# Performance work log

Measured on AMD Instinct MI355X. Metric: run time of the kernel, lower is better.

Reference implementation:

```python
import jax, jax.numpy as jnp
import numpy as np

B, N, H, OUT, L = 32, 4096, 256, 256, 4
EPS = 1e-5


def _build_edge_index(num_nodes):
    grid = int(np.sqrt(num_nodes)) + 1
    edges = []
    for i in range(num_nodes):
        col = i % grid
        if col < grid - 1 and i + 1 < num_nodes:
            edges.append([i, i + 1]); edges.append([i + 1, i])
        if i + grid < num_nodes:
            edges.append([i, i + grid]); edges.append([i + grid, i])
    return np.asarray(edges, dtype=np.int64).T  # [2, E]


def setup_inputs() -> dict:
    key = jax.random.key(0)
    ks = jax.random.split(key, 12)
    s = 0.02
    x = (jax.random.uniform(ks[0], (B, N)) < 0.1).astype(jnp.float32)  # syndrome bits
    edge_index = jnp.asarray(_build_edge_index(N))
    return {
        "x": x,
        "edge_index": edge_index,
        "proj_w": jax.random.normal(ks[1], (1, H)) * s,
        "proj_b": jnp.zeros((H,)),
        "conv_w": jax.random.normal(ks[2], (L, H, H)) * s,
        "conv_b": jnp.zeros((L, H)),
        "ln_g": jnp.ones((L, H)),
        "ln_b": jnp.zeros((L, H)),
        "h1_w": jax.random.normal(ks[3], (H, H)) * s,
        "h1_b": jnp.zeros((H,)),
        "h2_w": jax.random.normal(ks[4], (H, OUT)) * s,
        "h2_b": jnp.zeros((OUT,)),
    }


def reference(x, edge_index, proj_w, proj_b, conv_w, conv_b, ln_g, ln_b,
              h1_w, h1_b, h2_w, h2_b):
    batch, n = x.shape
    total = batch * n
    # batched edge index: replicate per sample with node offsets
    offsets = (jnp.arange(batch, dtype=edge_index.dtype) * n)
    ei = (edge_index[:, None, :] + offsets[None, :, None]).reshape(2, -1)
    src, dst = ei[0], ei[1]

    h = x.reshape(total, 1) @ proj_w + proj_b  # [total, H]

    # GCN symmetric norm with self-loops (degree = in-degree + 1)
    deg = jnp.zeros((total,), h.dtype).at[dst].add(1.0) + 1.0
    dinv_sqrt = jax.lax.rsqrt(deg)
    enorm = (dinv_sqrt[src] * dinv_sqrt[dst])[:, None]  # [E, 1]
    self_norm = (1.0 / deg)[:, None]                    # [total, 1]

    for l in range(L):
        t = h @ conv_w[l]                                   # transform
        agg = jnp.zeros_like(t).at[dst].add(enorm * t[src])  # scatter-add
        t = agg + self_norm * t + conv_b[l]
        mu = t.mean(-1, keepdims=True)
        var = ((t - mu) ** 2).mean(-1, keepdims=True)
        t = (t - mu) * jax.lax.rsqrt(var + EPS) * ln_g[l] + ln_b[l]
        h = jax.nn.relu(t)

    pooled = h.reshape(batch, n, -1).mean(axis=1)  # global_mean_pool (equal-size graphs)
    return jax.nn.relu(pooled @ h1_w + h1_b) @ h2_w + h2_b
```

## Files before the change

### kernel.cpp

```cpp
#include <hip/hip_runtime.h>
#include <cstdint>
#include <cstddef>

#define TOTAL (32*4096)
#define H 256
#define NLAYER 4

typedef _Float16 f16x8 __attribute__((ext_vector_type(8)));
typedef _Float16 f16x4 __attribute__((ext_vector_type(4)));
typedef float floatx4 __attribute__((ext_vector_type(4)));

__device__ __forceinline__ float dinv_of(int n) {
  int col = n % 65;
  int deg = 1;
  deg += (n >= 1 && col != 0) ? 1 : 0;
  deg += (col != 64 && n <= 4094) ? 1 : 0;
  deg += (n >= 65) ? 1 : 0;
  deg += (n <= 4030) ? 1 : 0;
  return rsqrtf((float)deg);
}

__device__ __forceinline__ void loadf8(const float* p, float* v) {
  float4 a = *reinterpret_cast<const float4*>(p);
  float4 b = *reinterpret_cast<const float4*>(p + 4);
  v[0] = a.x; v[1] = a.y; v[2] = a.z; v[3] = a.w;
  v[4] = b.x; v[5] = b.y; v[6] = b.z; v[7] = b.w;
}

__global__ void k_transpose(const float* __restrict__ src,
                            unsigned short* __restrict__ wt,
                            float* __restrict__ pooled) {
  int idx = blockIdx.x * 256 + threadIdx.x;
  if (blockIdx.x < 32) pooled[idx] = 0.0f;
  int n = idx & 255;
  int k = (idx >> 8) & 255;
  int l = idx >> 16;
  int wgrp = n >> 6, cc = n & 3, ll = (n >> 2) & 15;
  int ngrp = wgrp * 4 + cc;
  int c = k >> 5, lq = (k >> 3) & 3, j = k & 7;
  _Float16 hv = (_Float16)src[idx];
  union { _Float16 h; unsigned short u; } pk; pk.h = hv;
  wt[(size_t)l * 65536 + (ngrp * 8 + c) * 512 + (lq * 16 + ll) * 8 + j] = pk.u;
}

template <int AGG, int POOL, int GPROJ>
__global__ __launch_bounds__(256, 4)
void k_gemm_ln(const _Float16* __restrict__ Hin,
               const float* __restrict__ x,
               const float* __restrict__ pw,
               const float* __restrict__ pb,
               const _Float16* __restrict__ Bf,
               const float* __restrict__ cb,
               const float* __restrict__ lg,
               const float* __restrict__ lb,
               _Float16* __restrict__ Hout,
               float* __restrict__ pooled) {
  __shared__ alignas(16) unsigned char smem_u[64 * 130 * 4];
  _Float16* As = reinterpret_cast<_Float16*>(smem_u);
  float*    p2 = reinterpret_cast<float*>(smem_u);
  __shared__ float red2[4][64][2];
  __shared__ float musr[64][4];
  const int t = threadIdx.x;
  const int w = t >> 6, lane = t & 63;
  const int lq = lane >> 4, ll = lane & 15;
  const int tile = (blockIdx.x & 7) * (gridDim.x >> 3) + (blockIdx.x >> 3);
  const int m0 = tile * 64;
  const int wc = w * 64;
  const int ar = t >> 2;
  const int ak = (t & 3) * 8;

  {
    const int gi = m0 + ar;
    const int nd = gi & 4095;
    const int col = nd % 65;
    const float di = dinv_of(nd);
    if (GPROJ) {
      const int base = gi - nd;
      float sx = di * x[gi];
      float sc = di;
      if (nd >= 1 && col != 0)     { float dj = dinv_of(nd - 1);  sx += dj * x[base + nd - 1];  sc += dj; }
      if (col != 64 && nd <= 4094) { float dj = dinv_of(nd + 1);  sx += dj * x[base + nd + 1];  sc += dj; }
      if (nd >= 65)                { float dj = dinv_of(nd - 65); sx += dj * x[base + nd - 65]; sc += dj; }
      if (nd <= 4030)              { float dj = dinv_of(nd + 65); sx += dj * x[base + nd + 65]; sc += dj; }
      sx *= di; sc *= di;
#pragma unroll
      for (int c = 0; c < 8; c++) {
        const int k0 = c * 32 + ak;
        float wv[8], bv[8];
        loadf8(pw + k0, wv);
        loadf8(pb + k0, bv);
        f16x8 oh;
#pragma unroll
        for (int q = 0; q < 8; q++) oh[q] = (_Float16)(sx * wv[q] + sc * bv[q]);
        *reinterpret_cast<f16x8*>(&As[c * 2048 + ar * 32 + ak]) = oh;
      }
    } else if (AGG) {
      int j1 = gi, j2 = gi, j3 = gi, j4 = gi;
      _Float16 m1 = (_Float16)0.f, m2 = (_Float16)0.f, m3 = (_Float16)0.f, m4 = (_Float16)0.f;
      if (nd >= 1 && col != 0)     { j1 = gi - 1;  m1 = (_Float16)1.f; }
      if (col != 64 && nd <= 4094) { j2 = gi + 1;  m2 = (_Float16)1.f; }
      if (nd >= 65)                { j3 = gi - 65; m3 = (_Float16)1.f; }
      if (nd <= 4030)              { j4 = gi + 65; m4 = (_Float16)1.f; }
      const _Float16 dih = (_Float16)di;
      const _Float16* r0p = Hin + (size_t)gi * 256 + ak;
      const _Float16* r1p = Hin + (size_t)j1 * 256 + ak;
      const _Float16* r2p = Hin + (size_t)j2 * 256 + ak;
      const _Float16* r3p = Hin + (size_t)j3 * 256 + ak;
      const _Float16* r4p = Hin + (size_t)j4 * 256 + ak;
#pragma unroll
      for (int c = 0; c < 8; c++) {
        const int k0 = c * 32;
        f16x8 a0 = *reinterpret_cast<const f16x8*>(r0p + k0);
        f16x8 a1 = *reinterpret_cast<const f16x8*>(r1p + k0);
        f16x8 a2 = *reinterpret_cast<const f16x8*>(r2p + k0);
        f16x8 a3 = *reinterpret_cast<const f16x8*>(r3p + k0);
        f16x8 a4 = *reinterpret_cast<const f16x8*>(r4p + k0);
        f16x8 o = (a0 + a1 * m1 + a2 * m2 + a3 * m3 + a4 * m4) * dih;
        *reinterpret_cast<f16x8*>(&As[c * 2048 + ar * 32 + ak]) = o;
      }
    } else {
      const _Float16* r0p = Hin + (size_t)gi * 256 + ak;
#pragma unroll
      for (int c = 0; c < 8; c++)
        *reinterpret_cast<f16x8*>(&As[c * 2048 + ar * 32 + ak]) =
            *reinterpret_cast<const f16x8*>(r0p + c * 32);
    }
  }
  __syncthreads();

  floatx4 acc[4][4] = {};
  const _Float16* bbase = Bf + (size_t)(w * 4) * 8 * 512 + lane * 8;

#pragma unroll
  for (int c = 0; c < 8; c++) {
    f16x8 bfr[4], af[4];
#pragma unroll
    for (int cc = 0; cc < 4; cc++)
      bfr[cc] = *reinterpret_cast<const f16x8*>(bbase + (cc * 8 + c) * 512);
#pragma unroll
    for (int r = 0; r < 4; r++)
      af[r] = *reinterpret_cast<const f16x8*>(&As[c * 2048 + (r * 16 + ll) * 32 + lq * 8]);
#pragma unroll
    for (int r = 0; r < 4; r++)
#pragma unroll
      for (int cc = 0; cc < 4; cc++)
        acc[r][cc] = __builtin_amdgcn_mfma_f32_16x16x32_f16(af[r], bfr[cc], acc[r][cc], 0, 0, 0);
  }

  const int colbase = wc + (ll << 2);
  const float4 cb4 = *reinterpret_cast<const float4*>(cb + colbase);
  const float4 lg4 = *reinterpret_cast<const float4*>(lg + colbase);
  const float4 lb4 = *reinterpret_cast<const float4*>(lb + colbase);
  const float cbv[4]  = {cb4.x, cb4.y, cb4.z, cb4.w};
  const float gamv[4] = {lg4.x, lg4.y, lg4.z, lg4.w};
  const float betv[4] = {lb4.x, lb4.y, lb4.z, lb4.w};

  __syncthreads();
  {
    const int slice2 = (w * 16 + ll) * 2;
#pragma unroll
    for (int r = 0; r < 4; r++) {
#pragma unroll
      for (int reg = 0; reg < 4; reg++) {
        float sv = 0.f, sq = 0.f;
#pragma unroll
        for (int c = 0; c < 4; c++) {
          float v = acc[r][c][reg] + cbv[c];
          sv += v; sq += v * v;
        }
        const int row = r * 16 + lq * 4 + reg;
        *reinterpret_cast<float2*>(&p2[row * 130 + slice2]) = make_float2(sv, sq);
      }
    }
  }
  __syncthreads();
  {
    const int row = t & 63, qu = t >> 6;
    float s = 0.f, q = 0.f;
#pragma unroll
    for (int i = 0; i < 16; i++) {
      float2 pq = *reinterpret_cast<const float2*>(&p2[row * 130 + (qu * 16 + i) * 2]);
      s += pq.x; q += pq.y;
    }
    red2[qu][row][0] = s;
    red2[qu][row][1] = q;
  }
  __syncthreads();
  if (t < 64) {
    float s = red2[0][t][0] + red2[1][t][0] + red2[2][t][0] + red2[3][t][0];
    float q = red2[0][t][1] + red2[1][t][1] + red2[2][t][1] + red2[3][t][1];
    float mu = s * (1.0f / 256.0f);
    float var = fmaxf(q * (1.0f / 256.0f) - mu * mu, 0.0f);
    musr[t][0] = mu;
    musr[t][1] = rsqrtf(var + 1e-5f);
    musr[t][2] = dinv_of((m0 + t) & 4095);
  }
  __syncthreads();

  if (POOL == 0) {
#pragma unroll
    for (int r = 0; r < 4; r++) {
#pragma unroll
      for (int reg = 0; reg < 4; reg++) {
        int row = r * 16 + lq * 4 + reg;
        float mu = musr[row][0], rs = musr[row][1], dr = musr[row][2];
        f16x4 st;
#pragma unroll
        for (int c = 0; c < 4; c++) {
          float v = (acc[r][c][reg] + cbv[c] - mu) * rs * gamv[c] + betv[c];
          st[c] = (_Float16)(fmaxf(v, 0.0f) * dr);
        }
        *reinterpret_cast<f16x4*>(&Hout[(size_t)(m0 + row) * 256 + colbase]) = st;
      }
    }
  } else {
    float csum[4] = {0.f, 0.f, 0.f, 0.f};
#pragma unroll
    for (int r = 0; r < 4; r++) {
#pragma unroll
      for (int reg = 0; reg < 4; reg++) {
        int row = r * 16 + lq * 4 + reg;
        float mu = musr[row][0], rs = musr[row][1];
#pragma unroll
        for (int c = 0; c < 4; c++) {
          float hv = (acc[r][c][reg] + cbv[c] - mu) * rs * gamv[c] + betv[c];
          csum[c] += fmaxf(hv, 0.0f);
        }
      }
    }
#pragma unroll
    for (int c = 0; c < 4; c++) {
      csum[c] += __shfl_xor(csum[c], 16, 64);
      csum[c] += __shfl_xor(csum[c], 32, 64);
    }
    if (lq == 0) {
      int b = m0 >> 12;
#pragma unroll
      for (int c = 0; c < 4; c++)
        atomicAdd(&pooled[b * 256 + colbase + c], csum[c] * (1.0f / 4096.0f));
    }
  }
}

__global__ void k_head(const float* __restrict__ pooled,
                       const float* __restrict__ w1,
                       const float* __restrict__ b1,
                       const float* __restrict__ w2,
                       const float* __restrict__ b2,
                       float* __restrict__ out) {
  const int b = blockIdx.x;
  const int t = threadIdx.x;
  __shared__ float row[256];
  __shared__ float y1[256];
  row[t] = pooled[b * 256 + t];
  __syncthreads();
  float s = b1[t];
#pragma unroll 8
  for (int k = 0; k < 256; k++) s += row[k] * w1[k * 256 + t];
  y1[t] = fmaxf(s, 0.0f);
  __syncthreads();
  float s2 = b2[t];
#pragma unroll 8
  for (int k = 0; k < 256; k++) s2 += y1[k] * w2[k * 256 + t];
  out[b * 256 + t] = s2;
}

extern "C" void kernel_launch(void* const* d_in, const int* in_sizes, int n_in,
                              void* d_out, int out_size, void* d_ws, size_t ws_size,
                              hipStream_t stream) {
  (void)in_sizes; (void)n_in; (void)out_size; (void)ws_size;
  const float* x      = (const float*)d_in[0];
  const float* proj_w = (const float*)d_in[2];
  const float* proj_b = (const float*)d_in[3];
  const float* conv_w = (const float*)d_in[4];
  const float* conv_b = (const float*)d_in[5];
  const float* ln_g   = (const float*)d_in[6];
  const float* ln_b   = (const float*)d_in[7];
  const float* h1_w   = (const float*)d_in[8];
  const float* h1_b   = (const float*)d_in[9];
  const float* h2_w   = (const float*)d_in[10];
  const float* h2_b   = (const float*)d_in[11];

  char* ws = (char*)d_ws;
  const size_t act_bytes = (size_t)TOTAL * H * 2;
  _Float16* ha     = (_Float16*)ws;
  _Float16* hb     = (_Float16*)(ws + act_bytes);
  unsigned short* wt_u = (unsigned short*)(ws + 2 * act_bytes);
  _Float16* wt     = (_Float16*)wt_u;
  float*    pooled = (float*)(ws + 2 * act_bytes + (size_t)NLAYER * H * H * 2);

  k_transpose<<<NLAYER * H * H / 256, 256, 0, stream>>>(conv_w, wt_u, pooled);

  const int GB = TOTAL / 64;
  k_gemm_ln<0, 0, 1><<<GB, 256, 0, stream>>>(nullptr, x, proj_w, proj_b,
      wt + 0 * (size_t)H * H, conv_b + 0 * H, ln_g + 0 * H, ln_b + 0 * H, hb, nullptr);
  k_gemm_ln<1, 0, 0><<<GB, 256, 0, stream>>>(hb, nullptr, nullptr, nullptr,
      wt + 1 * (size_t)H * H, conv_b + 1 * H, ln_g + 1 * H, ln_b + 1 * H, ha, nullptr);
  k_gemm_ln<1, 0, 0><<<GB, 256, 0, stream>>>(ha, nullptr, nullptr, nullptr,
      wt + 2 * (size_t)H * H, conv_b + 2 * H, ln_g + 2 * H, ln_b + 2 * H, hb, nullptr);
  k_gemm_ln<1, 1, 0><<<GB, 256, 0, stream>>>(hb, nullptr, nullptr, nullptr,
      wt + 3 * (size_t)H * H, conv_b + 3 * H, ln_g + 3 * H, ln_b + 3 * H, nullptr, pooled);

  k_head<<<32, 256, 0, stream>>>(pooled, h1_w, h1_b, h2_w, h2_b, (float*)d_out);
}
```

Measured before the change: 273.5 us.

## Pipeline A-tile gather into double-buffered swizzled LDS inside the MFMA K-loop

Instead of gathering and aggregating the whole 64x256 A tile into shared memory before the GEMM, the kernel now keeps a two-stage LDS buffer of 32-wide K chunks. Global loads for chunk c+2 are issued during the MFMAs of chunk c, with a barrier each iteration. LDS rows are XOR-swizzled to cut bank conflicts, and launch bounds drop to 3 waves per SIMD to make room for the extra prefetch registers. The aim is to hide the neighbour-gather memory latency behind tensor-core work, at the cost of eight barriers per tile and lower occupancy.

```diff
diff --git a/kernel.cpp b/kernel.cpp
--- a/kernel.cpp
+++ b/kernel.cpp
@@ -18,13 +18,6 @@
   deg += (n >= 65) ? 1 : 0;
   deg += (n <= 4030) ? 1 : 0;
   return rsqrtf((float)deg);
-}
-
-__device__ __forceinline__ void loadf8(const float* p, float* v) {
-  float4 a = *reinterpret_cast<const float4*>(p);
-  float4 b = *reinterpret_cast<const float4*>(p + 4);
-  v[0] = a.x; v[1] = a.y; v[2] = a.z; v[3] = a.w;
-  v[4] = b.x; v[5] = b.y; v[6] = b.z; v[7] = b.w;
 }
 
 __global__ void k_transpose(const float* __restrict__ src,
@@ -44,7 +37,7 @@
 }
 
 template <int AGG, int POOL, int GPROJ>
-__global__ __launch_bounds__(256, 4)
+__global__ __launch_bounds__(256, 3)
 void k_gemm_ln(const _Float16* __restrict__ Hin,
                const float* __restrict__ x,
                const float* __restrict__ pw,
@@ -56,7 +49,7 @@
                _Float16* __restrict__ Hout,
                float* __restrict__ pooled) {
   __shared__ alignas(16) unsigned char smem_u[64 * 130 * 4];
-  _Float16* As = reinterpret_cast<_Float16*>(smem_u);
+  _Float16* Ad = reinterpret_cast<_Float16*>(smem_u);
   float*    p2 = reinterpret_cast<float*>(smem_u);
   __shared__ float red2[4][64][2];
   __shared__ float musr[64][4];
@@ -67,65 +60,77 @@
   const int m0 = tile * 64;
   const int wc = w * 64;
   const int ar = t >> 2;
-  const int ak = (t & 3) * 8;
-
-  {
-    const int gi = m0 + ar;
-    const int nd = gi & 4095;
-    const int col = nd % 65;
-    const float di = dinv_of(nd);
-    if (GPROJ) {
-      const int base = gi - nd;
-      float sx = di * x[gi];
-      float sc = di;
-      if (nd >= 1 && col != 0)     { float dj = dinv_of(nd - 1);  sx += dj * x[base + nd - 1];  sc += dj; }
-      if (col != 64 && nd <= 4094) { float dj = dinv_of(nd + 1);  sx += dj * x[base + nd + 1];  sc += dj; }
-      if (nd >= 65)                { float dj = dinv_of(nd - 65); sx += dj * x[base + nd - 65]; sc += dj; }
-      if (nd <= 4030)              { float dj = dinv_of(nd + 65); sx += dj * x[base + nd + 65]; sc += dj; }
-      sx *= di; sc *= di;
-#pragma unroll
-      for (int c = 0; c < 8; c++) {
-        const int k0 = c * 32 + ak;
-        float wv[8], bv[8];
-        loadf8(pw + k0, wv);
-        loadf8(pb + k0, bv);
-        f16x8 oh;
-#pragma unroll
-        for (int q = 0; q < 8; q++) oh[q] = (_Float16)(sx * wv[q] + sc * bv[q]);
-        *reinterpret_cast<f16x8*>(&As[c * 2048 + ar * 32 + ak]) = oh;
-      }
-    } else if (AGG) {
-      int j1 = gi, j2 = gi, j3 = gi, j4 = gi;
-      _Float16 m1 = (_Float16)0.f, m2 = (_Float16)0.f, m3 = (_Float16)0.f, m4 = (_Float16)0.f;
-      if (nd >= 1 && col != 0)     { j1 = gi - 1;  m1 = (_Float16)1.f; }
-      if (col != 64 && nd <= 4094) { j2 = gi + 1;  m2 = (_Float16)1.f; }
-      if (nd >= 65)                { j3 = gi - 65; m3 = (_Float16)1.f; }
-      if (nd <= 4030)              { j4 = gi + 65; m4 = (_Float16)1.f; }
-      const _Float16 dih = (_Float16)di;
-      const _Float16* r0p = Hin + (size_t)gi * 256 + ak;
-      const _Float16* r1p = Hin + (size_t)j1 * 256 + ak;
-      const _Float16* r2p = Hin + (size_t)j2 * 256 + ak;
-      const _Float16* r3p = Hin + (size_t)j3 * 256 + ak;
-      const _Float16* r4p = Hin + (size_t)j4 * 256 + ak;
-#pragma unroll
-      for (int c = 0; c < 8; c++) {
-        const int k0 = c * 32;
-        f16x8 a0 = *reinterpret_cast<const f16x8*>(r0p + k0);
-        f16x8 a1 = *reinterpret_cast<const f16x8*>(r1p + k0);
-        f16x8 a2 = *reinterpret_cast<const f16x8*>(r2p + k0);
-        f16x8 a3 = *reinterpret_cast<const f16x8*>(r3p + k0);
-        f16x8 a4 = *reinterpret_cast<const f16x8*>(r4p + k0);
-        f16x8 o = (a0 + a1 * m1 + a2 * m2 + a3 * m3 + a4 * m4) * dih;
-        *reinterpret_cast<f16x8*>(&As[c * 2048 + ar * 32 + ak]) = o;
-      }
-    } else {
-      const _Float16* r0p = Hin + (size_t)gi * 256 + ak;
-#pragma unroll
-      for (int c = 0; c < 8; c++)
-        *reinterpret_cast<f16x8*>(&As[c * 2048 + ar * 32 + ak]) =
-            *reinterpret_cast<const f16x8*>(r0p + c * 32);
-    }
-  }
+  const int slot = t & 3;
+  const int ak = slot * 8;
+  const int wpos = ar * 32 + ((slot ^ ((ar >> 1) & 3)) << 3);
+  const int rs   = ((lq ^ ((ll >> 1) & 3)) << 3);
+
+  const int gi = m0 + ar;
+  const int nd = gi & 4095;
+  const int col = nd % 65;
+  const float di = dinv_of(nd);
+
+  float sx = 0.f, sc = 0.f;
+  _Float16 m1 = (_Float16)0.f, m2 = (_Float16)0.f, m3 = (_Float16)0.f, m4 = (_Float16)0.f;
+  const _Float16 dih = (_Float16)di;
+  const _Float16* r0p = Hin + (size_t)gi * 256 + ak;
+  const _Float16* r1p = r0p;
+  const _Float16* r2p = r0p;
+  const _Float16* r3p = r0p;
+  const _Float16* r4p = r0p;
+  if (GPROJ) {
+    const int base = gi - nd;
+    sx = di * x[gi];
+    sc = di;
+    if (nd >= 1 && col != 0)     { float dj = dinv_of(nd - 1);  sx += dj * x[base + nd - 1];  sc += dj; }
+    if (col != 64 && nd <= 4094) { float dj = dinv_of(nd + 1);  sx += dj * x[base + nd + 1];  sc += dj; }
+    if (nd >= 65)                { float dj = dinv_of(nd - 65); sx += dj * x[base + nd - 65]; sc += dj; }
+    if (nd <= 4030)              { float dj = dinv_of(nd + 65); sx += dj * x[base + nd + 65]; sc += dj; }
+    sx *= di; sc *= di;
+  } else {
+    if (nd >= 1 && col != 0)     { r1p = r0p - 256;       m1 = (_Float16)1.f; }
+    if (col != 64 && nd <= 4094) { r2p = r0p + 256;       m2 = (_Float16)1.f; }
+    if (nd >= 65)                { r3p = r0p - 65 * 256;  m3 = (_Float16)1.f; }
+    if (nd <= 4030)              { r4p = r0p + 65 * 256;  m4 = (_Float16)1.f; }
+  }
+
+  f16x8 ga[2][5];
+  float4 gw[2][4];
+
+#define ISSUE(cc_, ss_)                                                          \
+  do { if ((cc_) < 8) {                                                          \
+    if (GPROJ) {                                                                 \
+      gw[ss_][0] = *reinterpret_cast<const float4*>(pw + (cc_) * 32 + ak);       \
+      gw[ss_][1] = *reinterpret_cast<const float4*>(pw + (cc_) * 32 + ak + 4);   \
+      gw[ss_][2] = *reinterpret_cast<const float4*>(pb + (cc_) * 32 + ak);       \
+      gw[ss_][3] = *reinterpret_cast<const float4*>(pb + (cc_) * 32 + ak + 4);   \
+    } else {                                                                     \
+      ga[ss_][0] = *reinterpret_cast<const f16x8*>(r0p + (cc_) * 32);            \
+      ga[ss_][1] = *reinterpret_cast<const f16x8*>(r1p + (cc_) * 32);            \
+      ga[ss_][2] = *reinterpret_cast<const f16x8*>(r2p + (cc_) * 32);            \
+      ga[ss_][3] = *reinterpret_cast<const f16x8*>(r3p + (cc_) * 32);            \
+      ga[ss_][4] = *reinterpret_cast<const f16x8*>(r4p + (cc_) * 32);            \
+    }                                                                            \
+  } } while (0)
+
+#define CWRITE(cc_, ss_)                                                         \
+  do { if ((cc_) < 8) {                                                          \
+    f16x8 o;                                                                     \
+    if (GPROJ) {                                                                 \
+      const float* wv = reinterpret_cast<const float*>(&gw[ss_][0]);             \
+      const float* bv = reinterpret_cast<const float*>(&gw[ss_][2]);             \
+      _Pragma("unroll")                                                          \
+      for (int q = 0; q < 8; q++) o[q] = (_Float16)(sx * wv[q] + sc * bv[q]);    \
+    } else {                                                                     \
+      o = (ga[ss_][0] + ga[ss_][1] * m1 + ga[ss_][2] * m2 +                      \
+           ga[ss_][3] * m3 + ga[ss_][4] * m4) * dih;                             \
+    }                                                                            \
+    *reinterpret_cast<f16x8*>(&Ad[((cc_) & 1) * 2048 + wpos]) = o;               \
+  } } while (0)
+
+  ISSUE(0, 0);
+  ISSUE(1, 1);
+  CWRITE(0, 0);
   __syncthreads();
 
   floatx4 acc[4][4] = {};
@@ -133,19 +138,25 @@
 
 #pragma unroll
   for (int c = 0; c < 8; c++) {
-    f16x8 bfr[4], af[4];
+    f16x8 bfr[4];
 #pragma unroll
     for (int cc = 0; cc < 4; cc++)
       bfr[cc] = *reinterpret_cast<const f16x8*>(bbase + (cc * 8 + c) * 512);
+    ISSUE(c + 2, ((c) & 1));
+    f16x8 af[4];
 #pragma unroll
     for (int r = 0; r < 4; r++)
-      af[r] = *reinterpret_cast<const f16x8*>(&As[c * 2048 + (r * 16 + ll) * 32 + lq * 8]);
+      af[r] = *reinterpret_cast<const f16x8*>(&Ad[(c & 1) * 2048 + (r * 16 + ll) * 32 + rs]);
 #pragma unroll
     for (int r = 0; r < 4; r++)
 #pragma unroll
       for (int cc = 0; cc < 4; cc++)
         acc[r][cc] = __builtin_amdgcn_mfma_f32_16x16x32_f16(af[r], bfr[cc], acc[r][cc], 0, 0, 0);
-  }
+    CWRITE(c + 1, ((c + 1) & 1));
+    __syncthreads();
+  }
+#undef ISSUE
+#undef CWRITE
 
   const int colbase = wc + (ll << 2);
   const float4 cb4 = *reinterpret_cast<const float4*>(cb + colbase);
@@ -155,7 +166,6 @@
   const float gamv[4] = {lg4.x, lg4.y, lg4.z, lg4.w};
   const float betv[4] = {lb4.x, lb4.y, lb4.z, lb4.w};
 
-  __syncthreads();
   {
     const int slice2 = (w * 16 + ll) * 2;
 #pragma unroll
@@ -203,11 +213,11 @@
 #pragma unroll
       for (int reg = 0; reg < 4; reg++) {
         int row = r * 16 + lq * 4 + reg;
-        float mu = musr[row][0], rs = musr[row][1], dr = musr[row][2];
+        float mu = musr[row][0], rsg = musr[row][1], dr = musr[row][2];
         f16x4 st;
 #pragma unroll
         for (int c = 0; c < 4; c++) {
-          float v = (acc[r][c][reg] + cbv[c] - mu) * rs * gamv[c] + betv[c];
+          float v = (acc[r][c][reg] + cbv[c] - mu) * rsg * gamv[c] + betv[c];
           st[c] = (_Float16)(fmaxf(v, 0.0f) * dr);
         }
         *reinterpret_cast<f16x4*>(&Hout[(size_t)(m0 + row) * 256 + colbase]) = st;
@@ -220,10 +230,10 @@
 #pragma unroll
       for (int reg = 0; reg < 4; reg++) {
         int row = r * 16 + lq * 4 + reg;
-        float mu = musr[row][0], rs = musr[row][1];
+        float mu = musr[row][0], rsg = musr[row][1];
 #pragma unroll
         for (int c = 0; c < 4; c++) {
-          float hv = (acc[r][c][reg] + cbv[c] - mu) * rs * gamv[c] + betv[c];
+          float hv = (acc[r][c][reg] + cbv[c] - mu) * rsg * gamv[c] + betv[c];
           csum[c] += fmaxf(hv, 0.0f);
         }
       }
```

Result: no change. 274.5 us (+0.4%).

## Split fused aggregate-GEMM-LN into separate GEMM and stencil+LayerNorm kernels

Applied to the files above, without the earlier changes.

Reorders each layer from aggregate-then-transform to transform-then-aggregate. A plain GEMM kernel writes Z = G·W, and a new stencil kernel performs the 5-point neighbour sum, bias, LayerNorm, ReLU and pooling. The stencil kernel writes its output already in MFMA fragment order, so the GEMM can copy A tiles directly into LDS, and the first layer now builds the projection inputs in registers. This removes the gather from the GEMM prologue and simplifies the LN reduction. The cost is an extra full activation round-trip through HBM and twice as many kernel launches.

```diff
diff --git a/kernel.cpp b/kernel.cpp
--- a/kernel.cpp
+++ b/kernel.cpp
@@ -26,6 +26,7 @@
   v[0] = a.x; v[1] = a.y; v[2] = a.z; v[3] = a.w;
   v[4] = b.x; v[5] = b.y; v[6] = b.z; v[7] = b.w;
 }
+
 
 __global__ void k_transpose(const float* __restrict__ src,
                             unsigned short* __restrict__ wt,
@@ -43,103 +44,65 @@
   wt[(size_t)l * 65536 + (ngrp * 8 + c) * 512 + (lq * 16 + ll) * 8 + j] = pk.u;
 }
 
-template <int AGG, int POOL, int GPROJ>
+template <int GPROJ>
 __global__ __launch_bounds__(256, 4)
-void k_gemm_ln(const _Float16* __restrict__ Hin,
-               const float* __restrict__ x,
-               const float* __restrict__ pw,
-               const float* __restrict__ pb,
-               const _Float16* __restrict__ Bf,
-               const float* __restrict__ cb,
-               const float* __restrict__ lg,
-               const float* __restrict__ lb,
-               _Float16* __restrict__ Hout,
-               float* __restrict__ pooled) {
-  __shared__ alignas(16) unsigned char smem_u[64 * 130 * 4];
-  _Float16* As = reinterpret_cast<_Float16*>(smem_u);
-  float*    p2 = reinterpret_cast<float*>(smem_u);
-  __shared__ float red2[4][64][2];
-  __shared__ float musr[64][4];
+void k_gemm(const _Float16* __restrict__ G,
+            const float* __restrict__ x,
+            const float* __restrict__ pw,
+            const float* __restrict__ pb,
+            const _Float16* __restrict__ Bf,
+            _Float16* __restrict__ Z) {
+  __shared__ alignas(16) unsigned char smem[32768];
+  _Float16* As = reinterpret_cast<_Float16*>(smem);
   const int t = threadIdx.x;
   const int w = t >> 6, lane = t & 63;
   const int lq = lane >> 4, ll = lane & 15;
   const int tile = (blockIdx.x & 7) * (gridDim.x >> 3) + (blockIdx.x >> 3);
   const int m0 = tile * 64;
-  const int wc = w * 64;
-  const int ar = t >> 2;
-  const int ak = (t & 3) * 8;
-
-  {
-    const int gi = m0 + ar;
-    const int nd = gi & 4095;
-    const int col = nd % 65;
-    const float di = dinv_of(nd);
+
+  float sxr[4], scr[4];
+  if (GPROJ) {
+#pragma unroll
+    for (int r = 0; r < 4; r++) {
+      int grow = m0 + r * 16 + ll;
+      float di = dinv_of(grow & 4095);
+      sxr[r] = di * x[grow];
+      scr[r] = di;
+    }
+  } else {
+    const uint4* gsrc = reinterpret_cast<const uint4*>(G + (size_t)m0 * 256);
+    uint4* ldst = reinterpret_cast<uint4*>(As);
+#pragma unroll
+    for (int i = 0; i < 8; i++)
+      ldst[i * 256 + t] = gsrc[i * 256 + t];
+    __syncthreads();
+  }
+
+  floatx4 acc[4][4] = {};
+  const _Float16* bbase = Bf + (size_t)(w * 4) * 8 * 512 + lane * 8;
+
+#pragma unroll
+  for (int c = 0; c < 8; c++) {
+    f16x8 bfr[4], af[4];
+#pragma unroll
+    for (int cc = 0; cc < 4; cc++)
+      bfr[cc] = *reinterpret_cast<const f16x8*>(bbase + (cc * 8 + c) * 512);
     if (GPROJ) {
-      const int base = gi - nd;
-      float sx = di * x[gi];
-      float sc = di;
-      if (nd >= 1 && col != 0)     { float dj = dinv_of(nd - 1);  sx += dj * x[base + nd - 1];  sc += dj; }
-      if (col != 64 && nd <= 4094) { float dj = dinv_of(nd + 1);  sx += dj * x[base + nd + 1];  sc += dj; }
-      if (nd >= 65)                { float dj = dinv_of(nd - 65); sx += dj * x[base + nd - 65]; sc += dj; }
-      if (nd <= 4030)              { float dj = dinv_of(nd + 65); sx += dj * x[base + nd + 65]; sc += dj; }
-      sx *= di; sc *= di;
-#pragma unroll
-      for (int c = 0; c < 8; c++) {
-        const int k0 = c * 32 + ak;
-        float wv[8], bv[8];
-        loadf8(pw + k0, wv);
-        loadf8(pb + k0, bv);
-        f16x8 oh;
-#pragma unroll
-        for (int q = 0; q < 8; q++) oh[q] = (_Float16)(sx * wv[q] + sc * bv[q]);
-        *reinterpret_cast<f16x8*>(&As[c * 2048 + ar * 32 + ak]) = oh;
-      }
-    } else if (AGG) {
-      int j1 = gi, j2 = gi, j3 = gi, j4 = gi;
-      _Float16 m1 = (_Float16)0.f, m2 = (_Float16)0.f, m3 = (_Float16)0.f, m4 = (_Float16)0.f;
-      if (nd >= 1 && col != 0)     { j1 = gi - 1;  m1 = (_Float16)1.f; }
-      if (col != 64 && nd <= 4094) { j2 = gi + 1;  m2 = (_Float16)1.f; }
-      if (nd >= 65)                { j3 = gi - 65; m3 = (_Float16)1.f; }
-      if (nd <= 4030)              { j4 = gi + 65; m4 = (_Float16)1.f; }
-      const _Float16 dih = (_Float16)di;
-      const _Float16* r0p = Hin + (size_t)gi * 256 + ak;
-      const _Float16* r1p = Hin + (size_t)j1 * 256 + ak;
-      const _Float16* r2p = Hin + (size_t)j2 * 256 + ak;
-      const _Float16* r3p = Hin + (size_t)j3 * 256 + ak;
-      const _Float16* r4p = Hin + (size_t)j4 * 256 + ak;
-#pragma unroll
-      for (int c = 0; c < 8; c++) {
-        const int k0 = c * 32;
-        f16x8 a0 = *reinterpret_cast<const f16x8*>(r0p + k0);
-        f16x8 a1 = *reinterpret_cast<const f16x8*>(r1p + k0);
-        f16x8 a2 = *reinterpret_cast<const f16x8*>(r2p + k0);
-        f16x8 a3 = *reinterpret_cast<const f16x8*>(r3p + k0);
-        f16x8 a4 = *reinterpret_cast<const f16x8*>(r4p + k0);
-        f16x8 o = (a0 + a1 * m1 + a2 * m2 + a3 * m3 + a4 * m4) * dih;
-        *reinterpret_cast<f16x8*>(&As[c * 2048 + ar * 32 + ak]) = o;
+      float wv[8], bv[8];
+      loadf8(pw + c * 32 + lq * 8, wv);
+      loadf8(pb + c * 32 + lq * 8, bv);
+#pragma unroll
+      for (int r = 0; r < 4; r++) {
+        f16x8 a;
+#pragma unroll
+        for (int j = 0; j < 8; j++) a[j] = (_Float16)(sxr[r] * wv[j] + scr[r] * bv[j]);
+        af[r] = a;
       }
     } else {
-      const _Float16* r0p = Hin + (size_t)gi * 256 + ak;
-#pragma unroll
-      for (int c = 0; c < 8; c++)
-        *reinterpret_cast<f16x8*>(&As[c * 2048 + ar * 32 + ak]) =
-            *reinterpret_cast<const f16x8*>(r0p + c * 32);
-    }
-  }
-  __syncthreads();
-
-  floatx4 acc[4][4] = {};
-  const _Float16* bbase = Bf + (size_t)(w * 4) * 8 * 512 + lane * 8;
-
-#pragma unroll
-  for (int c = 0; c < 8; c++) {
-    f16x8 bfr[4], af[4];
-#pragma unroll
-    for (int cc = 0; cc < 4; cc++)
-      bfr[cc] = *reinterpret_cast<const f16x8*>(bbase + (cc * 8 + c) * 512);
-#pragma unroll
-    for (int r = 0; r < 4; r++)
-      af[r] = *reinterpret_cast<const f16x8*>(&As[c * 2048 + (r * 16 + ll) * 32 + lq * 8]);
+#pragma unroll
+      for (int r = 0; r < 4; r++)
+        af[r] = *reinterpret_cast<const f16x8*>(&As[r * 4096 + c * 512 + lane * 8]);
+    }
 #pragma unroll
     for (int r = 0; r < 4; r++)
 #pragma unroll
@@ -147,98 +110,122 @@
         acc[r][cc] = __builtin_amdgcn_mfma_f32_16x16x32_f16(af[r], bfr[cc], acc[r][cc], 0, 0, 0);
   }
 
-  const int colbase = wc + (ll << 2);
-  const float4 cb4 = *reinterpret_cast<const float4*>(cb + colbase);
-  const float4 lg4 = *reinterpret_cast<const float4*>(lg + colbase);
-  const float4 lb4 = *reinterpret_cast<const float4*>(lb + colbase);
-  const float cbv[4]  = {cb4.x, cb4.y, cb4.z, cb4.w};
-  const float gamv[4] = {lg4.x, lg4.y, lg4.z, lg4.w};
-  const float betv[4] = {lb4.x, lb4.y, lb4.z, lb4.w};
-
-  __syncthreads();
-  {
-    const int slice2 = (w * 16 + ll) * 2;
-#pragma unroll
-    for (int r = 0; r < 4; r++) {
-#pragma unroll
-      for (int reg = 0; reg < 4; reg++) {
-        float sv = 0.f, sq = 0.f;
-#pragma unroll
-        for (int c = 0; c < 4; c++) {
-          float v = acc[r][c][reg] + cbv[c];
-          sv += v; sq += v * v;
-        }
-        const int row = r * 16 + lq * 4 + reg;
-        *reinterpret_cast<float2*>(&p2[row * 130 + slice2]) = make_float2(sv, sq);
-      }
-    }
-  }
-  __syncthreads();
-  {
-    const int row = t & 63, qu = t >> 6;
-    float s = 0.f, q = 0.f;
-#pragma unroll
-    for (int i = 0; i < 16; i++) {
-      float2 pq = *reinterpret_cast<const float2*>(&p2[row * 130 + (qu * 16 + i) * 2]);
-      s += pq.x; q += pq.y;
-    }
-    red2[qu][row][0] = s;
-    red2[qu][row][1] = q;
-  }
+  const int colbase = w * 64 + (ll << 2);
+#pragma unroll
+  for (int r = 0; r < 4; r++)
+#pragma unroll
+    for (int reg = 0; reg < 4; reg++) {
+      int row = m0 + r * 16 + lq * 4 + reg;
+      f16x4 st;
+#pragma unroll
+      for (int cc = 0; cc < 4; cc++) st[cc] = (_Float16)acc[r][cc][reg];
+      *reinterpret_cast<f16x4*>(&Z[(size_t)row * 256 + colbase]) = st;
+    }
+}
+
+template <int POOL>
+__global__ __launch_bounds__(256, 5)
+void k_stencil(const _Float16* __restrict__ Z,
+               const float* __restrict__ cb,
+               const float* __restrict__ lg,
+               const float* __restrict__ lb,
+               _Float16* __restrict__ Gout,
+               float* __restrict__ pooled) {
+  __shared__ float p2[256][2];
+  __shared__ float musr[64][2];
+  __shared__ float colsum[4][256];
+  const int t = threadIdx.x;
+  const int w = t >> 6, lane = t & 63;
+  const int gl = lane >> 2, s = lane & 3;
+  const int g = w * 16 + gl;
+  const int tile = (blockIdx.x & 7) * (gridDim.x >> 3) + (blockIdx.x >> 3);
+  const int m0 = tile * 64;
+  const int grow = m0 + g;
+  const int nd = grow & 4095;
+  const int col = nd % 65;
+  const float di = dinv_of(nd);
+
+  const _Float16* z0 = Z + (size_t)grow * 256 + s * 8;
+  const _Float16* z1 = z0; const _Float16* z2 = z0;
+  const _Float16* z3 = z0; const _Float16* z4 = z0;
+  _Float16 m1 = (_Float16)0.f, m2 = (_Float16)0.f, m3 = (_Float16)0.f, m4 = (_Float16)0.f;
+  if (nd >= 1 && col != 0)     { z1 = z0 - 256;      m1 = (_Float16)1.f; }
+  if (col != 64 && nd <= 4094) { z2 = z0 + 256;      m2 = (_Float16)1.f; }
+  if (nd >= 65)                { z3 = z0 - 65 * 256; m3 = (_Float16)1.f; }
+  if (nd <= 4030)              { z4 = z0 + 65 * 256; m4 = (_Float16)1.f; }
+
+  f16x8 tv[8];
+  float sv = 0.f, sq = 0.f;
+#pragma unroll
+  for (int mc = 0; mc < 8; mc++) {
+    const int k0 = mc * 32;
+    f16x8 a0 = *reinterpret_cast<const f16x8*>(z0 + k0);
+    f16x8 a1 = *reinterpret_cast<const f16x8*>(z1 + k0);
+    f16x8 a2 = *reinterpret_cast<const f16x8*>(z2 + k0);
+    f16x8 a3 = *reinterpret_cast<const f16x8*>(z3 + k0);
+    f16x8 a4 = *reinterpret_cast<const f16x8*>(z4 + k0);
+    f16x8 ssum = a0 + a1 * m1 + a2 * m2 + a3 * m3 + a4 * m4;
+    float cbv[8];
+    loadf8(cb + k0 + s * 8, cbv);
+    f16x8 th;
+#pragma unroll
+    for (int j = 0; j < 8; j++) {
+      float tj = di * (float)ssum[j] + cbv[j];
+      sv += tj; sq += tj * tj;
+      th[j] = (_Float16)tj;
+    }
+    tv[mc] = th;
+  }
+
+  p2[t][0] = sv; p2[t][1] = sq;
   __syncthreads();
   if (t < 64) {
-    float s = red2[0][t][0] + red2[1][t][0] + red2[2][t][0] + red2[3][t][0];
-    float q = red2[0][t][1] + red2[1][t][1] + red2[2][t][1] + red2[3][t][1];
-    float mu = s * (1.0f / 256.0f);
-    float var = fmaxf(q * (1.0f / 256.0f) - mu * mu, 0.0f);
+    float s0 = p2[t * 4][0] + p2[t * 4 + 1][0] + p2[t * 4 + 2][0] + p2[t * 4 + 3][0];
+    float q0 = p2[t * 4][1] + p2[t * 4 + 1][1] + p2[t * 4 + 2][1] + p2[t * 4 + 3][1];
+    float mu = s0 * (1.0f / 256.0f);
+    float var = fmaxf(q0 * (1.0f / 256.0f) - mu * mu, 0.0f);
     musr[t][0] = mu;
     musr[t][1] = rsqrtf(var + 1e-5f);
-    musr[t][2] = dinv_of((m0 + t) & 4095);
-  }
-  __syncthreads();
-
-  if (POOL == 0) {
-#pragma unroll
-    for (int r = 0; r < 4; r++) {
-#pragma unroll
-      for (int reg = 0; reg < 4; reg++) {
-        int row = r * 16 + lq * 4 + reg;
-        float mu = musr[row][0], rs = musr[row][1], dr = musr[row][2];
-        f16x4 st;
-#pragma unroll
-        for (int c = 0; c < 4; c++) {
-          float v = (acc[r][c][reg] + cbv[c] - mu) * rs * gamv[c] + betv[c];
-          st[c] = (_Float16)(fmaxf(v, 0.0f) * dr);
-        }
-        *reinterpret_cast<f16x4*>(&Hout[(size_t)(m0 + row) * 256 + colbase]) = st;
+  }
+  __syncthreads();
+  const float mu = musr[g][0], rs = musr[g][1];
+
+  const int R = grow >> 4, llg = grow & 15;
+#pragma unroll
+  for (int mc = 0; mc < 8; mc++) {
+    const int k0 = mc * 32;
+    float gv[8], bv[8];
+    loadf8(lg + k0 + s * 8, gv);
+    loadf8(lb + k0 + s * 8, bv);
+    float h[8];
+#pragma unroll
+    for (int j = 0; j < 8; j++) {
+      float v = ((float)tv[mc][j] - mu) * rs * gv[j] + bv[j];
+      h[j] = fmaxf(v, 0.0f);
+    }
+    if (POOL == 0) {
+      f16x8 o;
+#pragma unroll
+      for (int j = 0; j < 8; j++) o[j] = (_Float16)(h[j] * di);
+      *reinterpret_cast<f16x8*>(&Gout[(size_t)R * 4096 + mc * 512 + s * 128 + llg * 8]) = o;
+    } else {
+#pragma unroll
+      for (int j = 0; j < 8; j++) {
+        h[j] += __shfl_xor(h[j], 4, 64);
+        h[j] += __shfl_xor(h[j], 8, 64);
+        h[j] += __shfl_xor(h[j], 16, 64);
+        h[j] += __shfl_xor(h[j], 32, 64);
       }
-    }
-  } else {
-    float csum[4] = {0.f, 0.f, 0.f, 0.f};
-#pragma unroll
-    for (int r = 0; r < 4; r++) {
-#pragma unroll
-      for (int reg = 0; reg < 4; reg++) {
-        int row = r * 16 + lq * 4 + reg;
-        float mu = musr[row][0], rs = musr[row][1];
-#pragma unroll
-        for (int c = 0; c < 4; c++) {
-          float hv = (acc[r][c][reg] + cbv[c] - mu) * rs * gamv[c] + betv[c];
-          csum[c] += fmaxf(hv, 0.0f);
-        }
+      if (gl == 0) {
+        *reinterpret_cast<float4*>(&colsum[w][k0 + s * 8])     = make_float4(h[0], h[1], h[2], h[3]);
+        *reinterpret_cast<float4*>(&colsum[w][k0 + s * 8 + 4]) = make_float4(h[4], h[5], h[6], h[7]);
       }
     }
-#pragma unroll
-    for (int c = 0; c < 4; c++) {
-      csum[c] += __shfl_xor(csum[c], 16, 64);
-      csum[c] += __shfl_xor(csum[c], 32, 64);
-    }
-    if (lq == 0) {
-      int b = m0 >> 12;
-#pragma unroll
-      for (int c = 0; c < 4; c++)
-        atomicAdd(&pooled[b * 256 + colbase + c], csum[c] * (1.0f / 4096.0f));
-    }
+  }
+  if (POOL) {
+    __syncthreads();
+    float s4 = colsum[0][t] + colsum[1][t] + colsum[2][t] + colsum[3][t];
+    atomicAdd(&pooled[(m0 >> 12) * 256 + t], s4 * (1.0f / 4096.0f));
   }
 }
 
@@ -283,23 +270,24 @@
 
   char* ws = (char*)d_ws;
   const size_t act_bytes = (size_t)TOTAL * H * 2;
-  _Float16* ha     = (_Float16*)ws;
-  _Float16* hb     = (_Float16*)(ws + act_bytes);
-  unsigned short* wt_u = (unsigned short*)(ws + 2 * act_bytes);
-  _Float16* wt     = (_Float16*)wt_u;
-  float*    pooled = (float*)(ws + 2 * act_bytes + (size_t)NLAYER * H * H * 2);
+  _Float16* Zb  = (_Float16*)ws;
+  _Float16* Ga  = (_Float16*)(ws + act_bytes);
+  _Float16* Gb  = (_Float16*)(ws + 2 * act_bytes);
+  unsigned short* wt_u = (unsigned short*)(ws + 3 * act_bytes);
+  _Float16* wt  = (_Float16*)wt_u;
+  float*  pooled = (float*)(ws + 3 * act_bytes + (size_t)NLAYER * H * H * 2);
 
   k_transpose<<<NLAYER * H * H / 256, 256, 0, stream>>>(conv_w, wt_u, pooled);
 
   const int GB = TOTAL / 64;
-  k_gemm_ln<0, 0, 1><<<GB, 256, 0, stream>>>(nullptr, x, proj_w, proj_b,
-      wt + 0 * (size_t)H * H, conv_b + 0 * H, ln_g + 0 * H, ln_b + 0 * H, hb, nullptr);
-  k_gemm_ln<1, 0, 0><<<GB, 256, 0, stream>>>(hb, nullptr, nullptr, nullptr,
-      wt + 1 * (size_t)H * H, conv_b + 1 * H, ln_g + 1 * H, ln_b + 1 * H, ha, nullptr);
-  k_gemm_ln<1, 0, 0><<<GB, 256, 0, stream>>>(ha, nullptr, nullptr, nullptr,
-      wt + 2 * (size_t)H * H, conv_b + 2 * H, ln_g + 2 * H, ln_b + 2 * H, hb, nullptr);
-  k_gemm_ln<1, 1, 0><<<GB, 256, 0, stream>>>(hb, nullptr, nullptr, nullptr,
-      wt + 3 * (size_t)H * H, conv_b + 3 * H, ln_g + 3 * H, ln_b + 3 * H, nullptr, pooled);
+  k_gemm<1><<<GB, 256, 0, stream>>>(nullptr, x, proj_w, proj_b, wt + 0 * (size_t)H * H, Zb);
+  k_stencil<0><<<GB, 256, 0, stream>>>(Zb, conv_b + 0 * H, ln_g + 0 * H, ln_b + 0 * H, Ga, nullptr);
+  k_gemm<0><<<GB, 256, 0, stream>>>(Ga, nullptr, nullptr, nullptr, wt + 1 * (size_t)H * H, Zb);
+  k_stencil<0><<<GB, 256, 0, stream>>>(Zb, conv_b + 1 * H, ln_g + 1 * H, ln_b + 1 * H, Gb, nullptr);
+  k_gemm<0><<<GB, 256, 0, stream>>>(Gb, nullptr, nullptr, nullptr, wt + 2 * (size_t)H * H, Zb);
+  k_stencil<0><<<GB, 256, 0, stream>>>(Zb, conv_b + 2 * H, ln_g + 2 * H, ln_b + 2 * H, Ga, nullptr);
+  k_gemm<0><<<GB, 256, 0, stream>>>(Ga, nullptr, nullptr, nullptr, wt + 3 * (size_t)H * H, Zb);
+  k_stencil<1><<<GB, 256, 0, stream>>>(Zb, conv_b + 3 * H, ln_g + 3 * H, ln_b + 3 * H, nullptr, pooled);
 
   k_head<<<32, 256, 0, stream>>>(pooled, h1_w, h1_b, h2_w, h2_b, (float*)d_out);
 }
```

Measured after the change: 759.7 us. +177.8%, slower.

## Halve row tile to 32 and use padded row-major A tile in LDS

Applied to the files above, without the earlier changes.

Shrinks the per-block row tile from 64 to 32, doubling grid size, and changes the shared A tile from a k-chunked layout to a padded row-major layout (264 halves per row) with each thread loading a 32-wide k slice. Fewer accumulators per thread allow launch bounds of 5 blocks per CU, aiming for more occupancy and better latency hiding of the neighbour gathers. The cost is that each B fragment load now feeds half as many MFMAs, so weight traffic per output row doubles, and the LN reduction is reorganised into 8 partials per row.

```diff
diff --git a/kernel.cpp b/kernel.cpp
--- a/kernel.cpp
+++ b/kernel.cpp
@@ -44,7 +44,7 @@
 }
 
 template <int AGG, int POOL, int GPROJ>
-__global__ __launch_bounds__(256, 4)
+__global__ __launch_bounds__(256, 5)
 void k_gemm_ln(const _Float16* __restrict__ Hin,
                const float* __restrict__ x,
                const float* __restrict__ pw,
@@ -55,19 +55,20 @@
                const float* __restrict__ lb,
                _Float16* __restrict__ Hout,
                float* __restrict__ pooled) {
-  __shared__ alignas(16) unsigned char smem_u[64 * 130 * 4];
+  constexpr int ROWP = 264;
+  __shared__ alignas(16) unsigned char smem_u[32 * ROWP * 2];
   _Float16* As = reinterpret_cast<_Float16*>(smem_u);
   float*    p2 = reinterpret_cast<float*>(smem_u);
-  __shared__ float red2[4][64][2];
-  __shared__ float musr[64][4];
+  __shared__ float red2[8][32][2];
+  __shared__ float musr[32][4];
   const int t = threadIdx.x;
   const int w = t >> 6, lane = t & 63;
   const int lq = lane >> 4, ll = lane & 15;
   const int tile = (blockIdx.x & 7) * (gridDim.x >> 3) + (blockIdx.x >> 3);
-  const int m0 = tile * 64;
+  const int m0 = tile * 32;
   const int wc = w * 64;
-  const int ar = t >> 2;
-  const int ak = (t & 3) * 8;
+  const int ar = t >> 3;
+  const int ks = (t & 7) * 32;
 
   {
     const int gi = m0 + ar;
@@ -84,64 +85,57 @@
       if (nd <= 4030)              { float dj = dinv_of(nd + 65); sx += dj * x[base + nd + 65]; sc += dj; }
       sx *= di; sc *= di;
 #pragma unroll
-      for (int c = 0; c < 8; c++) {
-        const int k0 = c * 32 + ak;
+      for (int q = 0; q < 4; q++) {
+        const int k0 = ks + q * 8;
         float wv[8], bv[8];
         loadf8(pw + k0, wv);
         loadf8(pb + k0, bv);
         f16x8 oh;
 #pragma unroll
-        for (int q = 0; q < 8; q++) oh[q] = (_Float16)(sx * wv[q] + sc * bv[q]);
-        *reinterpret_cast<f16x8*>(&As[c * 2048 + ar * 32 + ak]) = oh;
-      }
-    } else if (AGG) {
-      int j1 = gi, j2 = gi, j3 = gi, j4 = gi;
+        for (int j = 0; j < 8; j++) oh[j] = (_Float16)(sx * wv[j] + sc * bv[j]);
+        *reinterpret_cast<f16x8*>(&As[ar * ROWP + k0]) = oh;
+      }
+    } else {
+      const _Float16 dih = (_Float16)di;
       _Float16 m1 = (_Float16)0.f, m2 = (_Float16)0.f, m3 = (_Float16)0.f, m4 = (_Float16)0.f;
-      if (nd >= 1 && col != 0)     { j1 = gi - 1;  m1 = (_Float16)1.f; }
-      if (col != 64 && nd <= 4094) { j2 = gi + 1;  m2 = (_Float16)1.f; }
-      if (nd >= 65)                { j3 = gi - 65; m3 = (_Float16)1.f; }
-      if (nd <= 4030)              { j4 = gi + 65; m4 = (_Float16)1.f; }
-      const _Float16 dih = (_Float16)di;
-      const _Float16* r0p = Hin + (size_t)gi * 256 + ak;
-      const _Float16* r1p = Hin + (size_t)j1 * 256 + ak;
-      const _Float16* r2p = Hin + (size_t)j2 * 256 + ak;
-      const _Float16* r3p = Hin + (size_t)j3 * 256 + ak;
-      const _Float16* r4p = Hin + (size_t)j4 * 256 + ak;
-#pragma unroll
-      for (int c = 0; c < 8; c++) {
-        const int k0 = c * 32;
+      const _Float16* r0p = Hin + (size_t)gi * 256 + ks;
+      const _Float16* r1p = r0p;
+      const _Float16* r2p = r0p;
+      const _Float16* r3p = r0p;
+      const _Float16* r4p = r0p;
+      if (nd >= 1 && col != 0)     { r1p = r0p - 256;      m1 = (_Float16)1.f; }
+      if (col != 64 && nd <= 4094) { r2p = r0p + 256;      m2 = (_Float16)1.f; }
+      if (nd >= 65)                { r3p = r0p - 65 * 256; m3 = (_Float16)1.f; }
+      if (nd <= 4030)              { r4p = r0p + 65 * 256; m4 = (_Float16)1.f; }
+#pragma unroll
+      for (int q = 0; q < 4; q++) {
+        const int k0 = q * 8;
         f16x8 a0 = *reinterpret_cast<const f16x8*>(r0p + k0);
         f16x8 a1 = *reinterpret_cast<const f16x8*>(r1p + k0);
         f16x8 a2 = *reinterpret_cast<const f16x8*>(r2p + k0);
         f16x8 a3 = *reinterpret_cast<const f16x8*>(r3p + k0);
         f16x8 a4 = *reinterpret_cast<const f16x8*>(r4p + k0);
         f16x8 o = (a0 + a1 * m1 + a2 * m2 + a3 * m3 + a4 * m4) * dih;
-        *reinterpret_cast<f16x8*>(&As[c * 2048 + ar * 32 + ak]) = o;
-      }
-    } else {
-      const _Float16* r0p = Hin + (size_t)gi * 256 + ak;
-#pragma unroll
-      for (int c = 0; c < 8; c++)
-        *reinterpret_cast<f16x8*>(&As[c * 2048 + ar * 32 + ak]) =
-            *reinterpret_cast<const f16x8*>(r0p + c * 32);
-    }
-  }
-  __syncthreads();
-
-  floatx4 acc[4][4] = {};
+        *reinterpret_cast<f16x8*>(&As[ar * ROWP + ks + k0]) = o;
+      }
+    }
+  }
+  __syncthreads();
+
+  floatx4 acc[2][4] = {};
   const _Float16* bbase = Bf + (size_t)(w * 4) * 8 * 512 + lane * 8;
 
 #pragma unroll
   for (int c = 0; c < 8; c++) {
-    f16x8 bfr[4], af[4];
+    f16x8 bfr[4], af[2];
 #pragma unroll
     for (int cc = 0; cc < 4; cc++)
       bfr[cc] = *reinterpret_cast<const f16x8*>(bbase + (cc * 8 + c) * 512);
 #pragma unroll
-    for (int r = 0; r < 4; r++)
-      af[r] = *reinterpret_cast<const f16x8*>(&As[c * 2048 + (r * 16 + ll) * 32 + lq * 8]);
-#pragma unroll
-    for (int r = 0; r < 4; r++)
+    for (int r = 0; r < 2; r++)
+      af[r] = *reinterpret_cast<const f16x8*>(&As[(r * 16 + ll) * ROWP + c * 32 + lq * 8]);
+#pragma unroll
+    for (int r = 0; r < 2; r++)
 #pragma unroll
       for (int cc = 0; cc < 4; cc++)
         acc[r][cc] = __builtin_amdgcn_mfma_f32_16x16x32_f16(af[r], bfr[cc], acc[r][cc], 0, 0, 0);
@@ -159,7 +153,7 @@
   {
     const int slice2 = (w * 16 + ll) * 2;
 #pragma unroll
-    for (int r = 0; r < 4; r++) {
+    for (int r = 0; r < 2; r++) {
 #pragma unroll
       for (int reg = 0; reg < 4; reg++) {
         float sv = 0.f, sq = 0.f;
@@ -175,20 +169,21 @@
   }
   __syncthreads();
   {
-    const int row = t & 63, qu = t >> 6;
+    const int row = t & 31, qu = t >> 5;
     float s = 0.f, q = 0.f;
 #pragma unroll
-    for (int i = 0; i < 16; i++) {
-      float2 pq = *reinterpret_cast<const float2*>(&p2[row * 130 + (qu * 16 + i) * 2]);
+    for (int i = 0; i < 8; i++) {
+      float2 pq = *reinterpret_cast<const float2*>(&p2[row * 130 + (qu * 8 + i) * 2]);
       s += pq.x; q += pq.y;
     }
     red2[qu][row][0] = s;
     red2[qu][row][1] = q;
   }
   __syncthreads();
-  if (t < 64) {
-    float s = red2[0][t][0] + red2[1][t][0] + red2[2][t][0] + red2[3][t][0];
-    float q = red2[0][t][1] + red2[1][t][1] + red2[2][t][1] + red2[3][t][1];
+  if (t < 32) {
+    float s = 0.f, q = 0.f;
+#pragma unroll
+    for (int o = 0; o < 8; o++) { s += red2[o][t][0]; q += red2[o][t][1]; }
     float mu = s * (1.0f / 256.0f);
     float var = fmaxf(q * (1.0f / 256.0f) - mu * mu, 0.0f);
     musr[t][0] = mu;
@@ -199,15 +194,15 @@
 
   if (POOL == 0) {
 #pragma unroll
-    for (int r = 0; r < 4; r++) {
+    for (int r = 0; r < 2; r++) {
 #pragma unroll
       for (int reg = 0; reg < 4; reg++) {
         int row = r * 16 + lq * 4 + reg;
-        float mu = musr[row][0], rs = musr[row][1], dr = musr[row][2];
+        float mu = musr[row][0], rsg = musr[row][1], dr = musr[row][2];
         f16x4 st;
 #pragma unroll
         for (int c = 0; c < 4; c++) {
-          float v = (acc[r][c][reg] + cbv[c] - mu) * rs * gamv[c] + betv[c];
+          float v = (acc[r][c][reg] + cbv[c] - mu) * rsg * gamv[c] + betv[c];
           st[c] = (_Float16)(fmaxf(v, 0.0f) * dr);
         }
         *reinterpret_cast<f16x4*>(&Hout[(size_t)(m0 + row) * 256 + colbase]) = st;
@@ -216,14 +211,14 @@
   } else {
     float csum[4] = {0.f, 0.f, 0.f, 0.f};
 #pragma unroll
-    for (int r = 0; r < 4; r++) {
+    for (int r = 0; r < 2; r++) {
 #pragma unroll
       for (int reg = 0; reg < 4; reg++) {
         int row = r * 16 + lq * 4 + reg;
-        float mu = musr[row][0], rs = musr[row][1];
+        float mu = musr[row][0], rsg = musr[row][1];
 #pragma unroll
         for (int c = 0; c < 4; c++) {
-          float hv = (acc[r][c][reg] + cbv[c] - mu) * rs * gamv[c] + betv[c];
+          float hv = (acc[r][c][reg] + cbv[c] - mu) * rsg * gamv[c] + betv[c];
           csum[c] += fmaxf(hv, 0.0f);
         }
       }
@@ -291,7 +286,7 @@
 
   k_transpose<<<NLAYER * H * H / 256, 256, 0, stream>>>(conv_w, wt_u, pooled);
 
-  const int GB = TOTAL / 64;
+  const int GB = TOTAL / 32;
   k_gemm_ln<0, 0, 1><<<GB, 256, 0, stream>>>(nullptr, x, proj_w, proj_b,
       wt + 0 * (size_t)H * H, conv_b + 0 * H, ln_g + 0 * H, ln_b + 0 * H, hb, nullptr);
   k_gemm_ln<1, 0, 0><<<GB, 256, 0, stream>>>(hb, nullptr, nullptr, nullptr,
```

New measurement: 337.5 us. +23.4%, slower.
